# Kernel optimization log

Hardware: AMD Instinct MI355X
Metric: run time of the kernel (lower is better)

## Reference

```python
import jax, jax.numpy as jnp
import numpy as np

N_NODES = 100_000
N_EDGES = 1_600_000
DIM = 64


def setup_inputs() -> dict:
    key = jax.random.key(0)
    ks = jax.random.split(key, 5)
    x = jax.random.normal(ks[0], (N_NODES, DIM), dtype=jnp.float32)
    edge_index = jax.random.randint(ks[1], (2, N_EDGES), 0, N_NODES, dtype=jnp.int64)
    scale = 1.0 / np.sqrt(DIM)
    W1 = jax.random.normal(ks[2], (DIM, DIM), dtype=jnp.float32) * scale
    b1 = jnp.zeros((DIM,), dtype=jnp.float32)
    W2 = jax.random.normal(ks[3], (DIM, DIM), dtype=jnp.float32) * scale
    b2 = jnp.zeros((DIM,), dtype=jnp.float32)
    return {"x": x, "edge_index": edge_index, "W1": W1, "b1": b1, "W2": W2, "b2": b2}


def reference(x, edge_index, W1, b1, W2, b2):
    # PyG GINEConv with edge_attr=None: message = relu(x_j) gathered over src edges
    src, dst = edge_index[0], edge_index[1]
    msg = jax.nn.relu(x[src])                                   # [E, dim] gather + relu
    agg = jax.ops.segment_sum(msg, dst, num_segments=x.shape[0])  # [N, dim] scatter-sum
    h = (1.0 + 0.0) * x + agg                                   # eps = 0 (train_eps=False)
    # gin_nn: Linear -> ReLU -> Linear
    h = jax.nn.relu(h @ W1 + b1) @ W2 + b2
    # outer F.relu; dropout is identity in eval mode
    return jax.nn.relu(h)
```

## Files before the change

kernel.cpp:

```cpp
#include <hip/hip_runtime.h>

#define N_NODES 100000
#define N_EDGES 1600000
#define DIM 64

#define BIN_SHIFT 9
#define BIN_NODES 512
#define NBINS ((N_NODES + BIN_NODES - 1) / BIN_NODES)
#define CAP 10240

#define TILE_A 8192
#define NBLK_A ((N_EDGES + TILE_A - 1) / TILE_A)
#define EPT (TILE_A / 512)

#define PREP_BLOCKS (N_NODES * DIM / 4 / 256)
#define WPREP_BLOCKS 32

typedef __attribute__((ext_vector_type(8))) short bf16x8;
typedef __attribute__((ext_vector_type(4))) float f32x4;

__device__ __forceinline__ float bflo(unsigned u) { return __uint_as_float(u << 16); }
__device__ __forceinline__ float bfhi(unsigned u) { return __uint_as_float(u & 0xFFFF0000u); }
__device__ __forceinline__ unsigned f2bf(float f) {
    unsigned u = __float_as_uint(f);
    u += 0x7FFFu + ((u >> 16) & 1u);
    return u >> 16;
}

__global__ __launch_bounds__(256) void prep_fused(
    const float* __restrict__ x, unsigned* __restrict__ rx,
    int* __restrict__ gcur,
    const float* __restrict__ W1, const float* __restrict__ W2,
    unsigned short* __restrict__ Wpk)
{
    const int blk = blockIdx.x;
    if (blk < PREP_BLOCKS) {
        if (blk == 0 && threadIdx.x < NBINS) gcur[threadIdx.x] = 0;
        const int i = blk * 256 + threadIdx.x;
        const float4 v = reinterpret_cast<const float4*>(x)[i];
        uint2 o;
        o.x = f2bf(fmaxf(v.x, 0.f)) | (f2bf(fmaxf(v.y, 0.f)) << 16);
        o.y = f2bf(fmaxf(v.z, 0.f)) | (f2bf(fmaxf(v.w, 0.f)) << 16);
        reinterpret_cast<uint2*>(rx)[i] = o;
    } else {
        const int idx = (blk - PREP_BLOCKS) * 256 + threadIdx.x;
        if (idx >= 8192) return;
        const int j    = idx & 7;
        const int lane = (idx >> 3) & 63;
        const int kk   = (idx >> 9) & 1;
        const int n    = (idx >> 10) & 3;
        const int L    = idx >> 12;
        const float* W = L ? W2 : W1;
        const int k    = kk * 32 + (lane >> 4) * 8 + j;
        const int col  = n * 16 + (lane & 15);
        Wpk[idx] = (unsigned short)f2bf(W[k * DIM + col]);
    }
}

__global__ __launch_bounds__(512) void binscatter(
    const int* __restrict__ ei,
    int* __restrict__ gcur,
    unsigned* __restrict__ binned)
{
    __shared__ int lhist[NBINS];
    __shared__ int lbase[NBINS];
    __shared__ int lcur[NBINS];
    __shared__ int ldelta[NBINS];
    __shared__ int ls[512];
    __shared__ unsigned staged[TILE_A];
    __shared__ unsigned char sbin[TILE_A];

    const int t  = threadIdx.x;
    const int e0 = blockIdx.x * TILE_A;
    const int n  = min(TILE_A, N_EDGES - e0);

    for (int i = t; i < NBINS; i += 512) { lhist[i] = 0; lcur[i] = 0; }
    __syncthreads();

    int      mybin[EPT];
    unsigned myval[EPT];
    #pragma unroll
    for (int q = 0; q < EPT / 4; ++q) {
        const int idx4 = q * 2048 + t * 4;
        if (idx4 < n) {
            const int4 s4 = *reinterpret_cast<const int4*>(ei + e0 + idx4);
            const int4 d4 = *reinterpret_cast<const int4*>(ei + N_EDGES + e0 + idx4);
            const int ss[4] = {s4.x, s4.y, s4.z, s4.w};
            const int dd[4] = {d4.x, d4.y, d4.z, d4.w};
            #pragma unroll
            for (int j = 0; j < 4; ++j) {
                mybin[q * 4 + j] = dd[j] >> BIN_SHIFT;
                myval[q * 4 + j] = ((unsigned)ss[j] << BIN_SHIFT)
                                 | (unsigned)(dd[j] & (BIN_NODES - 1));
                atomicAdd(&lhist[dd[j] >> BIN_SHIFT], 1);
            }
        } else {
            #pragma unroll
            for (int j = 0; j < 4; ++j) mybin[q * 4 + j] = -1;
        }
    }
    __syncthreads();

    ls[t] = (t < NBINS) ? lhist[t] : 0;
    __syncthreads();
    #pragma unroll
    for (int d = 1; d < 512; d <<= 1) {
        const int add = (t >= d) ? ls[t - d] : 0;
        __syncthreads();
        ls[t] += add;
        __syncthreads();
    }
    if (t < NBINS) lbase[t] = ls[t] - lhist[t];
    __syncthreads();

    if (t < NBINS) {
        const int c = lhist[t];
        ldelta[t] = (c > 0) ? (t * CAP + atomicAdd(&gcur[t], c) - lbase[t]) : 0;
    }
    __syncthreads();

    #pragma unroll
    for (int j = 0; j < EPT; ++j) {
        if (mybin[j] >= 0) {
            const int p = lbase[mybin[j]] + atomicAdd(&lcur[mybin[j]], 1);
            staged[p] = myval[j];
            sbin[p]   = (unsigned char)mybin[j];
        }
    }
    __syncthreads();

    for (int p = t; p < n; p += 512)
        binned[p + ldelta[sbin[p]]] = staged[p];
}

__global__ __launch_bounds__(256) void binsort(
    const unsigned* __restrict__ binned,
    const int* __restrict__ gcur,
    int* __restrict__ start,
    int* __restrict__ dega,
    int* __restrict__ slot)
{
    __shared__ int lhist[BIN_NODES];
    __shared__ int lofs[BIN_NODES];
    __shared__ int lcur[BIN_NODES];
    __shared__ int ls[256];
    __shared__ int sseg[CAP];

    const int b     = blockIdx.x;
    const int node0 = b << BIN_SHIFT;
    const int nloc  = min(BIN_NODES, N_NODES - node0);
    const int rbase = b * CAP;
    const int cnt   = min(gcur[b], CAP);
    const int t     = threadIdx.x;

    for (int i = t; i < BIN_NODES; i += 256) { lhist[i] = 0; lcur[i] = 0; }
    __syncthreads();

    for (int p = t; p < cnt; p += 256)
        atomicAdd(&lhist[binned[rbase + p] & (BIN_NODES - 1)], 1);
    __syncthreads();

    const int a0 = lhist[2 * t];
    const int a1 = lhist[2 * t + 1];
    const int ps = a0 + a1;
    ls[t] = ps;
    __syncthreads();
    #pragma unroll
    for (int d = 1; d < 256; d <<= 1) {
        const int add = (t >= d) ? ls[t - d] : 0;
        __syncthreads();
        ls[t] += add;
        __syncthreads();
    }
    const int pbase = ls[t] - ps;
    lofs[2 * t]     = pbase;
    lofs[2 * t + 1] = pbase + a0;
    __syncthreads();

    for (int i = t; i < nloc; i += 256) {
        start[node0 + i] = rbase + lofs[i];
        dega[node0 + i]  = lhist[i];
    }

    for (int p = t; p < cnt; p += 256) {
        const unsigned v = binned[rbase + p];
        const int dl  = v & (BIN_NODES - 1);
        const int rel = lofs[dl] + atomicAdd(&lcur[dl], 1);
        sseg[rel] = (int)(v >> BIN_SHIFT);
    }
    __syncthreads();
    for (int p = t; p < cnt; p += 256)
        slot[rbase + p] = sseg[p];
}

__global__ __launch_bounds__(512) void gather_mlp(
    const float* __restrict__ x,
    const unsigned char* __restrict__ rx,
    const int*   __restrict__ start,
    const int*   __restrict__ dega,
    const int*   __restrict__ slot,
    const unsigned short* __restrict__ Wpk,
    const float* __restrict__ b1,
    const float* __restrict__ b2,
    float* __restrict__ out)
{
    __shared__ unsigned ht[64 * 36];
    __shared__ float yt[4][16 * 68];

    const int t    = threadIdx.x;
    const int wv   = t >> 6;
    const int lane = t & 63;
    const int g    = lane >> 3;
    const int c    = lane & 7;
    const int row  = wv * 8 + g;
    const int node = blockIdx.x * 64 + row;

    uint4 o = make_uint4(0u, 0u, 0u, 0u);
    if (node < N_NODES) {
        const int beg = start[node];
        const int end = beg + dega[node];

        float acc[8];
        #pragma unroll
        for (int e = 0; e < 8; ++e) acc[e] = 0.f;

        for (int kb = beg; kb < end; kb += 8) {
            const int sv = (kb + c < end) ? slot[kb + c] : 0;

            int srcs[8];
            #pragma unroll
            for (int j = 0; j < 8; ++j) {
                const int s = __shfl(sv, g * 8 + j, 64);
                srcs[j] = (kb + j < end) ? s : 0;
            }
            uint4 buf[8];
            #pragma unroll
            for (int j = 0; j < 8; ++j)
                buf[j] = *reinterpret_cast<const uint4*>(
                    rx + (size_t)srcs[j] * 128 + c * 16);
            #pragma unroll
            for (int j = 0; j < 8; ++j) {
                if (kb + j < end) {
                    acc[0] += bflo(buf[j].x); acc[1] += bfhi(buf[j].x);
                    acc[2] += bflo(buf[j].y); acc[3] += bfhi(buf[j].y);
                    acc[4] += bflo(buf[j].z); acc[5] += bfhi(buf[j].z);
                    acc[6] += bflo(buf[j].w); acc[7] += bfhi(buf[j].w);
                }
            }
        }

        const float4 x0 = *reinterpret_cast<const float4*>(
            x + (size_t)node * DIM + c * 8);
        const float4 x1 = *reinterpret_cast<const float4*>(
            x + (size_t)node * DIM + c * 8 + 4);
        o.x = f2bf(x0.x + acc[0]) | (f2bf(x0.y + acc[1]) << 16);
        o.y = f2bf(x0.z + acc[2]) | (f2bf(x0.w + acc[3]) << 16);
        o.z = f2bf(x1.x + acc[4]) | (f2bf(x1.y + acc[5]) << 16);
        o.w = f2bf(x1.z + acc[6]) | (f2bf(x1.w + acc[7]) << 16);
    }
    *reinterpret_cast<uint4*>(&ht[row * 36 + c * 4]) = o;
    __syncthreads();

    if (wv >= 4) return;

    const int lrow = lane & 15;
    const int lgrp = lane >> 4;
    const int row2 = wv * 16 + lrow;

    union UF { uint4 u; bf16x8 v; };
    UF ha0, ha1;
    ha0.u = *reinterpret_cast<const uint4*>(&ht[row2 * 36 + lgrp * 4]);
    ha1.u = *reinterpret_cast<const uint4*>(&ht[row2 * 36 + 16 + lgrp * 4]);

    const uint4* wp = reinterpret_cast<const uint4*>(Wpk);

    float* my = &yt[wv][0];
    #pragma unroll
    for (int n = 0; n < 4; ++n) {
        const float bi = b1[n * 16 + lrow];
        f32x4 acc = {bi, bi, bi, bi};
        UF bw0, bw1;
        bw0.u = wp[(n * 2 + 0) * 64 + lane];
        bw1.u = wp[(n * 2 + 1) * 64 + lane];
        acc = __builtin_amdgcn_mfma_f32_16x16x32_bf16(ha0.v, bw0.v, acc, 0, 0, 0);
        acc = __builtin_amdgcn_mfma_f32_16x16x32_bf16(ha1.v, bw1.v, acc, 0, 0, 0);
        #pragma unroll
        for (int i = 0; i < 4; ++i)
            my[(lgrp * 4 + i) * 68 + n * 16 + lrow] = fmaxf(acc[i], 0.f);
    }

    const float* yr = &yt[wv][lrow * 68 + lgrp * 8];
    const float4 p0 = *reinterpret_cast<const float4*>(yr + 0);
    const float4 p1 = *reinterpret_cast<const float4*>(yr + 4);
    const float4 p2 = *reinterpret_cast<const float4*>(yr + 32);
    const float4 p3 = *reinterpret_cast<const float4*>(yr + 36);

    union UB { bf16x8 v; unsigned short s[8]; };
    UB ya0, ya1;
    ya0.s[0] = (unsigned short)f2bf(p0.x); ya0.s[1] = (unsigned short)f2bf(p0.y);
    ya0.s[2] = (unsigned short)f2bf(p0.z); ya0.s[3] = (unsigned short)f2bf(p0.w);
    ya0.s[4] = (unsigned short)f2bf(p1.x); ya0.s[5] = (unsigned short)f2bf(p1.y);
    ya0.s[6] = (unsigned short)f2bf(p1.z); ya0.s[7] = (unsigned short)f2bf(p1.w);
    ya1.s[0] = (unsigned short)f2bf(p2.x); ya1.s[1] = (unsigned short)f2bf(p2.y);
    ya1.s[2] = (unsigned short)f2bf(p2.z); ya1.s[3] = (unsigned short)f2bf(p2.w);
    ya1.s[4] = (unsigned short)f2bf(p3.x); ya1.s[5] = (unsigned short)f2bf(p3.y);
    ya1.s[6] = (unsigned short)f2bf(p3.z); ya1.s[7] = (unsigned short)f2bf(p3.w);

    #pragma unroll
    for (int n = 0; n < 4; ++n) {
        const float bi = b2[n * 16 + lrow];
        f32x4 acc = {bi, bi, bi, bi};
        UF bw0, bw1;
        bw0.u = wp[(8 + n * 2 + 0) * 64 + lane];
        bw1.u = wp[(8 + n * 2 + 1) * 64 + lane];
        acc = __builtin_amdgcn_mfma_f32_16x16x32_bf16(ya0.v, bw0.v, acc, 0, 0, 0);
        acc = __builtin_amdgcn_mfma_f32_16x16x32_bf16(ya1.v, bw1.v, acc, 0, 0, 0);
        #pragma unroll
        for (int i = 0; i < 4; ++i) {
            const int r = blockIdx.x * 64 + wv * 16 + lgrp * 4 + i;
            if (r < N_NODES)
                out[(size_t)r * DIM + n * 16 + lrow] = fmaxf(acc[i], 0.f);
        }
    }
}

extern "C" void kernel_launch(void* const* d_in, const int* in_sizes, int n_in,
                              void* d_out, int out_size, void* d_ws, size_t ws_size,
                              hipStream_t stream) {
    const float* x  = (const float*)d_in[0];
    const int*   ei = (const int*)d_in[1];
    const float* W1 = (const float*)d_in[2];
    const float* b1 = (const float*)d_in[3];
    const float* W2 = (const float*)d_in[4];
    const float* b2 = (const float*)d_in[5];
    float* out = (float*)d_out;

    int* start = (int*)d_ws;
    int* dega  = start + 100352;
    int* gcur  = dega + 100352;
    int* slot  = gcur + 256;
    unsigned* binned = (unsigned*)(slot + NBINS * CAP);
    unsigned* rx     = binned + NBINS * CAP;
    unsigned short* Wpk =
        (unsigned short*)(rx + (size_t)N_NODES * 32);

    prep_fused<<<PREP_BLOCKS + WPREP_BLOCKS, 256, 0, stream>>>(
        x, rx, gcur, W1, W2, Wpk);

    binscatter<<<NBLK_A, 512, 0, stream>>>(ei, gcur, binned);
    binsort<<<NBINS, 256, 0, stream>>>(binned, gcur, start, dega, slot);

    gather_mlp<<<(N_NODES + 63) / 64, 512, 0, stream>>>(
        x, (const unsigned char*)rx, start, dega, slot, Wpk, b1, b2, out);
}
```

Baseline: 80.49 us.

## Fuse edge binning into prep kernel and replace global bin atomics with per-tile tables

Merges the edge-binning scatter into the prep launch, which removes one kernel launch and the global atomic cursor. Each tile now writes its binned edges contiguously plus per-bin count and offset tables. The sort kernel walks these tables serially per tile (196 tiles spread over 256 threads) instead of reading a contiguous bin segment. The gather-MLP kernel is resized to 32 nodes per 256-thread block with bounds checks dropped, since 100000 divides evenly by 32. The trade-off is that the sort becomes serial per tile, with scattered small reads and poor thread utilization.

```diff
diff --git a/kernel.cpp b/kernel.cpp
--- a/kernel.cpp
+++ b/kernel.cpp
@@ -13,8 +13,9 @@
 #define NBLK_A ((N_EDGES + TILE_A - 1) / TILE_A)
 #define EPT (TILE_A / 512)
 
-#define PREP_BLOCKS (N_NODES * DIM / 4 / 256)
-#define WPREP_BLOCKS 32
+#define SCAT_BLOCKS  NBLK_A
+#define PREP_BLOCKS  (N_NODES * DIM / 4 / 512)
+#define WPREP_BLOCKS 16
 
 typedef __attribute__((ext_vector_type(8))) short bf16x8;
 typedef __attribute__((ext_vector_type(4))) float f32x4;
@@ -27,23 +28,93 @@
     return u >> 16;
 }
 
-__global__ __launch_bounds__(256) void prep_fused(
+__global__ __launch_bounds__(512) void prep_scatter(
     const float* __restrict__ x, unsigned* __restrict__ rx,
-    int* __restrict__ gcur,
     const float* __restrict__ W1, const float* __restrict__ W2,
-    unsigned short* __restrict__ Wpk)
+    unsigned short* __restrict__ Wpk,
+    const int* __restrict__ ei,
+    unsigned* __restrict__ binned,
+    int* __restrict__ tblc, int* __restrict__ tblb)
 {
+    __shared__ int lhist[NBINS];
+    __shared__ int lbase[NBINS];
+    __shared__ int lcur[NBINS];
+    __shared__ int ls[512];
+    __shared__ unsigned staged[TILE_A];
+
+    const int t   = threadIdx.x;
     const int blk = blockIdx.x;
-    if (blk < PREP_BLOCKS) {
-        if (blk == 0 && threadIdx.x < NBINS) gcur[threadIdx.x] = 0;
-        const int i = blk * 256 + threadIdx.x;
+
+    if (blk < SCAT_BLOCKS) {
+        const int e0 = blk * TILE_A;
+        const int n  = min(TILE_A, N_EDGES - e0);
+
+        for (int i = t; i < NBINS; i += 512) { lhist[i] = 0; lcur[i] = 0; }
+        __syncthreads();
+
+        int      mybin[EPT];
+        unsigned myval[EPT];
+        #pragma unroll
+        for (int q = 0; q < EPT / 4; ++q) {
+            const int idx4 = q * 2048 + t * 4;
+            if (idx4 < n) {
+                const int4 s4 = *reinterpret_cast<const int4*>(ei + e0 + idx4);
+                const int4 d4 = *reinterpret_cast<const int4*>(ei + N_EDGES + e0 + idx4);
+                const int ss[4] = {s4.x, s4.y, s4.z, s4.w};
+                const int dd[4] = {d4.x, d4.y, d4.z, d4.w};
+                #pragma unroll
+                for (int j = 0; j < 4; ++j) {
+                    mybin[q * 4 + j] = dd[j] >> BIN_SHIFT;
+                    myval[q * 4 + j] = ((unsigned)ss[j] << BIN_SHIFT)
+                                     | (unsigned)(dd[j] & (BIN_NODES - 1));
+                    atomicAdd(&lhist[dd[j] >> BIN_SHIFT], 1);
+                }
+            } else {
+                #pragma unroll
+                for (int j = 0; j < 4; ++j) mybin[q * 4 + j] = -1;
+            }
+        }
+        __syncthreads();
+
+        ls[t] = (t < NBINS) ? lhist[t] : 0;
+        __syncthreads();
+        #pragma unroll
+        for (int d = 1; d < 512; d <<= 1) {
+            const int add = (t >= d) ? ls[t - d] : 0;
+            __syncthreads();
+            ls[t] += add;
+            __syncthreads();
+        }
+        if (t < NBINS) lbase[t] = ls[t] - lhist[t];
+        __syncthreads();
+
+        for (int i = t; i < NBINS; i += 512) {
+            tblc[blk * NBINS + i] = lhist[i];
+            tblb[blk * NBINS + i] = lbase[i];
+        }
+
+        #pragma unroll
+        for (int j = 0; j < EPT; ++j) {
+            if (mybin[j] >= 0) {
+                const int p = lbase[mybin[j]] + atomicAdd(&lcur[mybin[j]], 1);
+                staged[p] = myval[j];
+            }
+        }
+        __syncthreads();
+
+        for (int p = t; p < n; p += 512)
+            binned[e0 + p] = staged[p];
+
+    } else if (blk < SCAT_BLOCKS + PREP_BLOCKS) {
+        const int i = (blk - SCAT_BLOCKS) * 512 + t;
         const float4 v = reinterpret_cast<const float4*>(x)[i];
         uint2 o;
         o.x = f2bf(fmaxf(v.x, 0.f)) | (f2bf(fmaxf(v.y, 0.f)) << 16);
         o.y = f2bf(fmaxf(v.z, 0.f)) | (f2bf(fmaxf(v.w, 0.f)) << 16);
         reinterpret_cast<uint2*>(rx)[i] = o;
+
     } else {
-        const int idx = (blk - PREP_BLOCKS) * 256 + threadIdx.x;
+        const int idx = (blk - SCAT_BLOCKS - PREP_BLOCKS) * 512 + t;
         if (idx >= 8192) return;
         const int j    = idx & 7;
         const int lane = (idx >> 3) & 63;
@@ -57,85 +128,9 @@
     }
 }
 
-__global__ __launch_bounds__(512) void binscatter(
-    const int* __restrict__ ei,
-    int* __restrict__ gcur,
-    unsigned* __restrict__ binned)
-{
-    __shared__ int lhist[NBINS];
-    __shared__ int lbase[NBINS];
-    __shared__ int lcur[NBINS];
-    __shared__ int ldelta[NBINS];
-    __shared__ int ls[512];
-    __shared__ unsigned staged[TILE_A];
-    __shared__ unsigned char sbin[TILE_A];
-
-    const int t  = threadIdx.x;
-    const int e0 = blockIdx.x * TILE_A;
-    const int n  = min(TILE_A, N_EDGES - e0);
-
-    for (int i = t; i < NBINS; i += 512) { lhist[i] = 0; lcur[i] = 0; }
-    __syncthreads();
-
-    int      mybin[EPT];
-    unsigned myval[EPT];
-    #pragma unroll
-    for (int q = 0; q < EPT / 4; ++q) {
-        const int idx4 = q * 2048 + t * 4;
-        if (idx4 < n) {
-            const int4 s4 = *reinterpret_cast<const int4*>(ei + e0 + idx4);
-            const int4 d4 = *reinterpret_cast<const int4*>(ei + N_EDGES + e0 + idx4);
-            const int ss[4] = {s4.x, s4.y, s4.z, s4.w};
-            const int dd[4] = {d4.x, d4.y, d4.z, d4.w};
-            #pragma unroll
-            for (int j = 0; j < 4; ++j) {
-                mybin[q * 4 + j] = dd[j] >> BIN_SHIFT;
-                myval[q * 4 + j] = ((unsigned)ss[j] << BIN_SHIFT)
-                                 | (unsigned)(dd[j] & (BIN_NODES - 1));
-                atomicAdd(&lhist[dd[j] >> BIN_SHIFT], 1);
-            }
-        } else {
-            #pragma unroll
-            for (int j = 0; j < 4; ++j) mybin[q * 4 + j] = -1;
-        }
-    }
-    __syncthreads();
-
-    ls[t] = (t < NBINS) ? lhist[t] : 0;
-    __syncthreads();
-    #pragma unroll
-    for (int d = 1; d < 512; d <<= 1) {
-        const int add = (t >= d) ? ls[t - d] : 0;
-        __syncthreads();
-        ls[t] += add;
-        __syncthreads();
-    }
-    if (t < NBINS) lbase[t] = ls[t] - lhist[t];
-    __syncthreads();
-
-    if (t < NBINS) {
-        const int c = lhist[t];
-        ldelta[t] = (c > 0) ? (t * CAP + atomicAdd(&gcur[t], c) - lbase[t]) : 0;
-    }
-    __syncthreads();
-
-    #pragma unroll
-    for (int j = 0; j < EPT; ++j) {
-        if (mybin[j] >= 0) {
-            const int p = lbase[mybin[j]] + atomicAdd(&lcur[mybin[j]], 1);
-            staged[p] = myval[j];
-            sbin[p]   = (unsigned char)mybin[j];
-        }
-    }
-    __syncthreads();
-
-    for (int p = t; p < n; p += 512)
-        binned[p + ldelta[sbin[p]]] = staged[p];
-}
-
 __global__ __launch_bounds__(256) void binsort(
     const unsigned* __restrict__ binned,
-    const int* __restrict__ gcur,
+    const int* __restrict__ tblc, const int* __restrict__ tblb,
     int* __restrict__ start,
     int* __restrict__ dega,
     int* __restrict__ slot)
@@ -150,14 +145,17 @@
     const int node0 = b << BIN_SHIFT;
     const int nloc  = min(BIN_NODES, N_NODES - node0);
     const int rbase = b * CAP;
-    const int cnt   = min(gcur[b], CAP);
     const int t     = threadIdx.x;
 
     for (int i = t; i < BIN_NODES; i += 256) { lhist[i] = 0; lcur[i] = 0; }
     __syncthreads();
 
-    for (int p = t; p < cnt; p += 256)
-        atomicAdd(&lhist[binned[rbase + p] & (BIN_NODES - 1)], 1);
+    for (int sb = t; sb < NBLK_A; sb += 256) {
+        const int cnt  = tblc[sb * NBINS + b];
+        const int base = sb * TILE_A + tblb[sb * NBINS + b];
+        for (int i = 0; i < cnt; ++i)
+            atomicAdd(&lhist[binned[base + i] & (BIN_NODES - 1)], 1);
+    }
     __syncthreads();
 
     const int a0 = lhist[2 * t];
@@ -177,23 +175,30 @@
     lofs[2 * t + 1] = pbase + a0;
     __syncthreads();
 
+    const int total = min(lofs[BIN_NODES - 1] + lhist[BIN_NODES - 1], CAP);
+
     for (int i = t; i < nloc; i += 256) {
         start[node0 + i] = rbase + lofs[i];
         dega[node0 + i]  = lhist[i];
     }
 
-    for (int p = t; p < cnt; p += 256) {
-        const unsigned v = binned[rbase + p];
-        const int dl  = v & (BIN_NODES - 1);
-        const int rel = lofs[dl] + atomicAdd(&lcur[dl], 1);
-        sseg[rel] = (int)(v >> BIN_SHIFT);
-    }
-    __syncthreads();
-    for (int p = t; p < cnt; p += 256)
+    for (int sb = t; sb < NBLK_A; sb += 256) {
+        const int cnt  = tblc[sb * NBINS + b];
+        const int base = sb * TILE_A + tblb[sb * NBINS + b];
+        for (int i = 0; i < cnt; ++i) {
+            const unsigned v = binned[base + i];
+            const int dl  = v & (BIN_NODES - 1);
+            const int rel = lofs[dl] + atomicAdd(&lcur[dl], 1);
+            if (rel < CAP) sseg[rel] = (int)(v >> BIN_SHIFT);
+        }
+    }
+    __syncthreads();
+
+    for (int p = t; p < total; p += 256)
         slot[rbase + p] = sseg[p];
 }
 
-__global__ __launch_bounds__(512) void gather_mlp(
+__global__ __launch_bounds__(256) void gather_mlp(
     const float* __restrict__ x,
     const unsigned char* __restrict__ rx,
     const int*   __restrict__ start,
@@ -204,8 +209,8 @@
     const float* __restrict__ b2,
     float* __restrict__ out)
 {
-    __shared__ unsigned ht[64 * 36];
-    __shared__ float yt[4][16 * 68];
+    __shared__ unsigned ht[32 * 36];
+    __shared__ float yt[2][16 * 68];
 
     const int t    = threadIdx.x;
     const int wv   = t >> 6;
@@ -213,10 +218,9 @@
     const int g    = lane >> 3;
     const int c    = lane & 7;
     const int row  = wv * 8 + g;
-    const int node = blockIdx.x * 64 + row;
-
-    uint4 o = make_uint4(0u, 0u, 0u, 0u);
-    if (node < N_NODES) {
+    const int node = blockIdx.x * 32 + row;
+
+    {
         const int beg = start[node];
         const int end = beg + dega[node];
 
@@ -253,15 +257,16 @@
             x + (size_t)node * DIM + c * 8);
         const float4 x1 = *reinterpret_cast<const float4*>(
             x + (size_t)node * DIM + c * 8 + 4);
+        uint4 o;
         o.x = f2bf(x0.x + acc[0]) | (f2bf(x0.y + acc[1]) << 16);
         o.y = f2bf(x0.z + acc[2]) | (f2bf(x0.w + acc[3]) << 16);
         o.z = f2bf(x1.x + acc[4]) | (f2bf(x1.y + acc[5]) << 16);
         o.w = f2bf(x1.z + acc[6]) | (f2bf(x1.w + acc[7]) << 16);
-    }
-    *reinterpret_cast<uint4*>(&ht[row * 36 + c * 4]) = o;
-    __syncthreads();
-
-    if (wv >= 4) return;
+        *reinterpret_cast<uint4*>(&ht[row * 36 + c * 4]) = o;
+    }
+    __syncthreads();
+
+    if (wv >= 2) return;
 
     const int lrow = lane & 15;
     const int lgrp = lane >> 4;
@@ -315,12 +320,10 @@
         bw1.u = wp[(8 + n * 2 + 1) * 64 + lane];
         acc = __builtin_amdgcn_mfma_f32_16x16x32_bf16(ya0.v, bw0.v, acc, 0, 0, 0);
         acc = __builtin_amdgcn_mfma_f32_16x16x32_bf16(ya1.v, bw1.v, acc, 0, 0, 0);
-        #pragma unroll
-        for (int i = 0; i < 4; ++i) {
-            const int r = blockIdx.x * 64 + wv * 16 + lgrp * 4 + i;
-            if (r < N_NODES)
-                out[(size_t)r * DIM + n * 16 + lrow] = fmaxf(acc[i], 0.f);
-        }
+        const int r = blockIdx.x * 32 + wv * 16 + lgrp * 4;
+        #pragma unroll
+        for (int i = 0; i < 4; ++i)
+            out[(size_t)(r + i) * DIM + n * 16 + lrow] = fmaxf(acc[i], 0.f);
     }
 }
 
@@ -337,19 +340,19 @@
 
     int* start = (int*)d_ws;
     int* dega  = start + 100352;
-    int* gcur  = dega + 100352;
-    int* slot  = gcur + 256;
+    int* tblc  = dega + 100352;
+    int* tblb  = tblc + 40960;
+    int* slot  = tblb + 40960;
     unsigned* binned = (unsigned*)(slot + NBINS * CAP);
-    unsigned* rx     = binned + NBINS * CAP;
+    unsigned* rx     = binned + NBLK_A * TILE_A;
     unsigned short* Wpk =
         (unsigned short*)(rx + (size_t)N_NODES * 32);
 
-    prep_fused<<<PREP_BLOCKS + WPREP_BLOCKS, 256, 0, stream>>>(
-        x, rx, gcur, W1, W2, Wpk);
-
-    binscatter<<<NBLK_A, 512, 0, stream>>>(ei, gcur, binned);
-    binsort<<<NBINS, 256, 0, stream>>>(binned, gcur, start, dega, slot);
-
-    gather_mlp<<<(N_NODES + 63) / 64, 512, 0, stream>>>(
+    prep_scatter<<<SCAT_BLOCKS + PREP_BLOCKS + WPREP_BLOCKS, 512, 0, stream>>>(
+        x, rx, W1, W2, Wpk, ei, binned, tblc, tblb);
+
+    binsort<<<NBINS, 256, 0, stream>>>(binned, tblc, tblb, start, dega, slot);
+
+    gather_mlp<<<3125, 256, 0, stream>>>(
         x, (const unsigned char*)rx, start, dega, slot, Wpk, b1, b2, out);
 }
```

Result: faster. 72.05 us (-10.5%).
